# Kernel tuning notes

Measured on AMD Instinct MI355X. Metric: run time of the kernel, lower is better.

The kernel has to match this reference:

```python
import jax, jax.numpy as jnp
import numpy as np
import math

B, S, H, NH, NB = 2, 512, 128, 4, 2
D = H // NH
V_ITEMS, NCAT, NMETA, BAG, TSPAN = 50000, 1000, 16, 5, 256
EPS_EMB, EPS = 1e-5, 1e-8
NEG = -(2.0 ** 32) + 1.0


def _ln(x, g, b, eps):
    m = x.mean(-1, keepdims=True)
    v = ((x - m) ** 2).mean(-1, keepdims=True)
    return (x - m) / jnp.sqrt(v + eps) * g + b


def setup_inputs() -> dict:
    key = jax.random.key(0)
    ks = jax.random.split(key, 24)
    sc = 0.02
    inp = {}
    inp['input_ids'] = jax.random.randint(ks[0], (B, S), 0, V_ITEMS + 1)
    inp['metadata_seq'] = jax.random.normal(ks[1], (B, S, NMETA), jnp.float32)
    inp['category_seq'] = jax.random.randint(ks[2], (B, S, BAG), 0, NCAT + 1)
    inp['time_matrix'] = jax.random.randint(ks[3], (B, S, S), 0, TSPAN + 1)
    item = jax.random.normal(ks[4], (V_ITEMS + 1, H), jnp.float32) * sc
    inp['item_emb_w'] = item.at[0].set(0.0)  # padding_idx=0 cleared
    cat = jax.random.normal(ks[5], (NCAT + 1, H // 2), jnp.float32) * sc
    inp['cat_emb_w'] = cat.at[0].set(0.0)
    inp['num_W'] = jax.random.normal(ks[6], (H // 2, NMETA), jnp.float32) * sc
    inp['num_b'] = jnp.zeros((H // 2,), jnp.float32)
    inp['fusion_W'] = jax.random.normal(ks[7], (H, 2 * H), jnp.float32) * sc
    inp['fusion_b'] = jnp.zeros((H,), jnp.float32)
    inp['emb_ln_g'] = jnp.ones((H,), jnp.float32)
    inp['emb_ln_b'] = jnp.zeros((H,), jnp.float32)
    inp['pos_K_w'] = jax.random.normal(ks[8], (S, H), jnp.float32) * sc
    inp['pos_V_w'] = jax.random.normal(ks[9], (S, H), jnp.float32) * sc
    inp['time_K_w'] = jax.random.normal(ks[10], (TSPAN + 1, H), jnp.float32) * sc
    inp['time_V_w'] = jax.random.normal(ks[11], (TSPAN + 1, H), jnp.float32) * sc
    inp['attn_ln_g'] = jnp.ones((NB, H), jnp.float32)
    inp['attn_ln_b'] = jnp.zeros((NB, H), jnp.float32)
    inp['Q_W'] = jax.random.normal(ks[12], (NB, H, H), jnp.float32) * sc
    inp['Q_b'] = jnp.zeros((NB, H), jnp.float32)
    inp['K_W'] = jax.random.normal(ks[13], (NB, H, H), jnp.float32) * sc
    inp['K_b'] = jnp.zeros((NB, H), jnp.float32)
    inp['V_W'] = jax.random.normal(ks[14], (NB, H, H), jnp.float32) * sc
    inp['V_b'] = jnp.zeros((NB, H), jnp.float32)
    inp['fwd_ln_g'] = jnp.ones((NB, H), jnp.float32)
    inp['fwd_ln_b'] = jnp.zeros((NB, H), jnp.float32)
    inp['w1_W'] = jax.random.normal(ks[15], (NB, H, H), jnp.float32) * sc
    inp['w1_b'] = jnp.zeros((NB, H), jnp.float32)
    inp['w2_W'] = jax.random.normal(ks[16], (NB, H, H), jnp.float32) * sc
    inp['w2_b'] = jnp.zeros((NB, H), jnp.float32)
    inp['last_ln_g'] = jnp.ones((H,), jnp.float32)
    inp['last_ln_b'] = jnp.zeros((H,), jnp.float32)
    return inp


def reference(input_ids, metadata_seq, category_seq, time_matrix, item_emb_w,
              cat_emb_w, num_W, num_b, fusion_W, fusion_b, emb_ln_g, emb_ln_b,
              pos_K_w, pos_V_w, time_K_w, time_V_w, attn_ln_g, attn_ln_b,
              Q_W, Q_b, K_W, K_b, V_W, V_b, fwd_ln_g, fwd_ln_b,
              w1_W, w1_b, w2_W, w2_b, last_ln_g, last_ln_b):
    # ---- seq2vec ----
    item_v = item_emb_w[input_ids] * math.sqrt(H)            # [B,S,H]
    bag_mask = (category_seq != 0)                           # EmbeddingBag mean, padding_idx=0
    cat_e = cat_emb_w[category_seq] * bag_mask[..., None]    # [B,S,BAG,H/2]
    cat_v = cat_e.sum(-2) / jnp.maximum(bag_mask.sum(-1, keepdims=True), 1)
    num_v = metadata_seq @ num_W.T + num_b                   # [B,S,H/2]
    comb = jnp.concatenate([item_v, num_v, cat_v], axis=-1)  # [B,S,2H]
    vecs = _ln(comb @ fusion_W.T + fusion_b, emb_ln_g, emb_ln_b, EPS_EMB)

    # ---- vec2feats ----
    posK = pos_K_w.reshape(S, NH, D)
    posV = pos_V_w.reshape(S, NH, D)
    tK = time_K_w[time_matrix].reshape(B, S, S, NH, D)       # [B,S,S,h,d]
    tV = time_V_w[time_matrix].reshape(B, S, S, NH, D)
    timeline = (input_ids == 0)                              # [B,S]
    keep = (~timeline)[..., None].astype(vecs.dtype)
    vecs = vecs * keep
    causal = ~jnp.tril(jnp.ones((S, S), bool))               # mask where j > i
    inv_sqrt_d = 1.0 / math.sqrt(D)

    for i in range(NB):
        Qn = _ln(vecs, attn_ln_g[i], attn_ln_b[i], EPS)
        Q = (Qn @ Q_W[i].T + Q_b[i]).reshape(B, S, NH, D)
        K = (vecs @ K_W[i].T + K_b[i]).reshape(B, S, NH, D)
        V = (vecs @ V_W[i].T + V_b[i]).reshape(B, S, NH, D)
        aw = jnp.einsum('bihd,bjhd->bhij', Q, K)
        aw = aw + jnp.einsum('bihd,jhd->bhij', Q, posK)
        aw = aw + jnp.einsum('bijhd,bihd->bhij', tK, Q)
        aw = aw * inv_sqrt_d
        aw = jnp.where(timeline[:, None, :, None], NEG, aw)  # masks query rows (as in torch)
        aw = jnp.where(causal[None, None], NEG, aw)
        aw = jax.nn.softmax(aw, axis=-1)
        out = jnp.einsum('bhij,bjhd->bihd', aw, V)
        out = out + jnp.einsum('bhij,jhd->bihd', aw, posV)
        out = out + jnp.einsum('bhij,bijhd->bihd', aw, tV)
        out = out.reshape(B, S, H)
        vecs = Qn + out
        vecs = _ln(vecs, fwd_ln_g[i], fwd_ln_b[i], EPS)
        h1 = jax.nn.gelu(vecs @ w1_W[i].T + w1_b[i], approximate=False)
        vecs = vecs + (h1 @ w2_W[i].T + w2_b[i])
        vecs = vecs * keep

    return _ln(vecs, last_ln_g, last_ln_b, EPS)
```

## Files before the change

### kernel.cpp

```cpp
#include <hip/hip_runtime.h>
#include <math.h>

#define Bn 2
#define Sn 512
#define Hn 128
#define NHn 4
#define Dn 32
#define BAGn 5
#define NMETAn 16
#define ROWS 1024
#define NBn 2
#define Tt 257

#define NEGF (-4294967295.0f)
#define INV_SQRT_D 0.17677669529663687f
#define SQRT_H 11.313708498984761f
#define EPS_EMB 1e-5f
#define EPSF 1e-8f

#define OFF_QN    0
#define OFF_Q     131072
#define OFF_K     262144
#define OFF_V     393216
#define OFF_O     524288

static __device__ __forceinline__ float red64(float v) {
#pragma unroll
    for (int m = 1; m < 64; m <<= 1) v += __shfl_xor(v, m, 64);
    return v;
}
static __device__ __forceinline__ float red64max(float v) {
#pragma unroll
    for (int m = 1; m < 64; m <<= 1) v = fmaxf(v, __shfl_xor(v, m, 64));
    return v;
}
static __device__ __forceinline__ float dot4(float4 a, float4 b) {
    return a.x * b.x + a.y * b.y + a.z * b.z + a.w * b.w;
}
static __device__ __forceinline__ float red4(float v) {
    v += __shfl_xor(v, 1, 64);
    v += __shfl_xor(v, 2, 64);
    return v;
}

__global__ __launch_bounds__(256) void embed_qkv_kernel(
    const int* __restrict__ ids, const float* __restrict__ meta,
    const int* __restrict__ cats,
    const float* __restrict__ item_w, const float* __restrict__ cat_w,
    const float* __restrict__ numW, const float* __restrict__ numb,
    const float* __restrict__ fusW, const float* __restrict__ fusb,
    const float* __restrict__ elng, const float* __restrict__ elnb,
    const float* __restrict__ alng, const float* __restrict__ alnb,
    const float* __restrict__ QW, const float* __restrict__ Qb,
    const float* __restrict__ KW, const float* __restrict__ Kb,
    const float* __restrict__ VW, const float* __restrict__ Vb,
    const float* __restrict__ posK, const float* __restrict__ posV,
    const int* __restrict__ tmat, const float* __restrict__ tKw,
    const float* __restrict__ tVw,
    float* __restrict__ Qn, float* __restrict__ Q,
    float* __restrict__ K, float* __restrict__ V)
{
    int r0 = blockIdx.x * 2, t = threadIdx.x;
    __shared__ __align__(16) float combs[512];
    __shared__ __align__(16) float xs[256];
    __shared__ __align__(16) float qs[256];
    __shared__ float wsum[8];
    __shared__ int idl[2];

    int pfi = 0; float pff = 0.f;
    {
        const int* tm = tmat + blockIdx.x * 1024;
#pragma unroll
        for (int j = 0; j < 4; ++j) pfi += tm[t + j * 256];
        if (t < 64) {
            int off = blockIdx.x * 64 + t;
            pff = tKw[off] + tVw[off];
        } else if (blockIdx.x == 0 && t < 192) {
            pff = tKw[32704 + t] + tVw[32704 + t];
        }
    }

    if (t < 2) idl[t] = ids[r0 + t];
    __syncthreads();
    { int r = t >> 7, c = t & 127; combs[r * 256 + c] = item_w[idl[r] * Hn + c] * SQRT_H; }
    if (t < 128) {
        int r = t >> 6, c = t & 63;
        const float4* m4 = (const float4*)(meta + (r0 + r) * NMETAn);
        const float4* w4 = (const float4*)(numW + c * NMETAn);
        float acc = numb[c];
#pragma unroll
        for (int j = 0; j < 4; ++j) acc += dot4(m4[j], w4[j]);
        combs[r * 256 + 128 + c] = acc;
    } else {
        int u = t - 128, r = u >> 6, c = u & 63;
        float ca = 0.f; int cnt = 0;
#pragma unroll
        for (int k2 = 0; k2 < BAGn; ++k2) {
            int cc2 = cats[(r0 + r) * BAGn + k2];
            if (cc2 != 0) { ca += cat_w[cc2 * 64 + c]; cnt++; }
        }
        combs[r * 256 + 192 + c] = ca / (float)(cnt > 0 ? cnt : 1);
    }
    asm volatile("" :: "v"(pfi), "v"(pff));
    __syncthreads();

    int q = t & 3, g = t >> 2;
#pragma unroll
    for (int p = 0; p < 2; ++p) {
        int h = p * 64 + g;
        const float4* w4 = (const float4*)(fusW + h * 256) + q;
        const float4* c0 = (const float4*)(combs) + q;
        const float4* c1 = (const float4*)(combs + 256) + q;
        float a0 = 0.f, a1 = 0.f;
#pragma unroll
        for (int j = 0; j < 16; ++j) {
            float4 w = w4[j * 4];
            a0 += dot4(c0[j * 4], w);
            a1 += dot4(c1[j * 4], w);
        }
        a0 = red4(a0); a1 = red4(a1);
        if (q == 0)      xs[h]       = a0 + fusb[h];
        else if (q == 1) xs[128 + h] = a1 + fusb[h];
    }
    __syncthreads();

    int w_ = t >> 6, row = w_ >> 1, l = t & 63, ch = ((w_ & 1) << 6) + l;
    float x = xs[row * 128 + ch];
    float s1 = red64(x);
    if (l == 0) wsum[w_] = s1;
    __syncthreads();
    float mean = (wsum[row * 2] + wsum[row * 2 + 1]) * (1.f / 128.f);
    float dlt = x - mean;
    float s2 = red64(dlt * dlt);
    if (l == 0) wsum[4 + w_] = s2;
    __syncthreads();
    float rstd = rsqrtf((wsum[4 + row * 2] + wsum[4 + row * 2 + 1]) * (1.f / 128.f) + EPS_EMB);
    float xv = dlt * rstd * elng[ch] + elnb[ch];
    xv = (idl[row] == 0) ? 0.f : xv;
    __syncthreads();
    xs[row * 128 + ch] = xv;
    __syncthreads();
    s1 = red64(xv);
    if (l == 0) wsum[w_] = s1;
    __syncthreads();
    mean = (wsum[row * 2] + wsum[row * 2 + 1]) * (1.f / 128.f);
    dlt = xv - mean;
    s2 = red64(dlt * dlt);
    if (l == 0) wsum[4 + w_] = s2;
    __syncthreads();
    rstd = rsqrtf((wsum[4 + row * 2] + wsum[4 + row * 2 + 1]) * (1.f / 128.f) + EPSF);
    float qn = dlt * rstd * alng[ch] + alnb[ch];
    qs[row * 128 + ch] = qn;
    Qn[(r0 + row) * 128 + ch] = qn;
    __syncthreads();

#pragma unroll
    for (int p = 0; p < 2; ++p) {
        int h = p * 64 + g;
        const float4* qw = (const float4*)(QW + h * 128) + q;
        const float4* kw = (const float4*)(KW + h * 128) + q;
        const float4* vw = (const float4*)(VW + h * 128) + q;
        const float4* s0p = (const float4*)(qs) + q;
        const float4* s1p = (const float4*)(qs + 128) + q;
        const float4* x0p = (const float4*)(xs) + q;
        const float4* x1p = (const float4*)(xs + 128) + q;
        float aq0 = 0, aq1 = 0, ak0 = 0, ak1 = 0, av0 = 0, av1 = 0;
#pragma unroll
        for (int j = 0; j < 8; ++j) {
            float4 wq = qw[j * 4], wk = kw[j * 4], wv = vw[j * 4];
            float4 u0 = s0p[j * 4], u1 = s1p[j * 4];
            float4 y0 = x0p[j * 4], y1 = x1p[j * 4];
            aq0 += dot4(u0, wq); aq1 += dot4(u1, wq);
            ak0 += dot4(y0, wk); ak1 += dot4(y1, wk);
            av0 += dot4(y0, wv); av1 += dot4(y1, wv);
        }
        aq0 = red4(aq0); aq1 = red4(aq1);
        ak0 = red4(ak0); ak1 = red4(ak1);
        av0 = red4(av0); av1 = red4(av1);
        if (q == 0) {
            int si = r0 & (Sn - 1);
            Q[r0 * Hn + h] = aq0 + Qb[h];
            K[r0 * Hn + h] = ak0 + Kb[h] + posK[si * Hn + h];
            V[r0 * Hn + h] = av0 + Vb[h] + posV[si * Hn + h];
        } else if (q == 1) {
            int si = (r0 + 1) & (Sn - 1);
            Q[(r0 + 1) * Hn + h] = aq1 + Qb[h];
            K[(r0 + 1) * Hn + h] = ak1 + Kb[h] + posK[si * Hn + h];
            V[(r0 + 1) * Hn + h] = av1 + Vb[h] + posV[si * Hn + h];
        }
    }
}

static __device__ __forceinline__ void attn_phase(
    int b, int h, int i0, int t,
    const int* __restrict__ ids, const int* __restrict__ tmat,
    const float* __restrict__ Q, const float* __restrict__ K,
    const float* __restrict__ V,
    const float* __restrict__ tKw, const float* __restrict__ tVw,
    float* __restrict__ O,
    float* Kt, float* Vt, float* Stile, int* trowT,
    float* QTl, float* ql, int* tlf)
{
    if (t < 4) tlf[t] = (ids[b * Sn + i0 + t] == 0) ? 1 : 0;
    if (t < 128) {
        int q_ = t >> 5, d = t & 31;
        ql[q_ * 36 + d] = Q[(b * Sn + i0 + q_) * Hn + h * 32 + d];
    }
    __syncthreads();

    {
        int qq = t & 3, gg = t >> 2;
#pragma unroll
        for (int c = 0; c < 4; ++c) {
            int tt = c * 64 + gg;
            const float4* tk4 = (const float4*)(tKw + tt * Hn + h * 32);
            float4 wA = tk4[qq];
            float4 wB = tk4[qq + 4];
            int dA = qq * 4, dB = 16 + qq * 4;
            float a0 = ql[dA]*wA.x + ql[dA+1]*wA.y + ql[dA+2]*wA.z + ql[dA+3]*wA.w
                     + ql[dB]*wB.x + ql[dB+1]*wB.y + ql[dB+2]*wB.z + ql[dB+3]*wB.w;
            float a1 = ql[36+dA]*wA.x + ql[37+dA]*wA.y + ql[38+dA]*wA.z + ql[39+dA]*wA.w
                     + ql[36+dB]*wB.x + ql[37+dB]*wB.y + ql[38+dB]*wB.z + ql[39+dB]*wB.w;
            float a2 = ql[72+dA]*wA.x + ql[73+dA]*wA.y + ql[74+dA]*wA.z + ql[75+dA]*wA.w
                     + ql[72+dB]*wB.x + ql[73+dB]*wB.y + ql[74+dB]*wB.z + ql[75+dB]*wB.w;
            float a3 = ql[108+dA]*wA.x + ql[109+dA]*wA.y + ql[110+dA]*wA.z + ql[111+dA]*wA.w
                     + ql[108+dB]*wB.x + ql[109+dB]*wB.y + ql[110+dB]*wB.z + ql[111+dB]*wB.w;
            a0 = red4(a0); a1 = red4(a1); a2 = red4(a2); a3 = red4(a3);
            if (qq == 0)      QTl[tt] = a0;
            else if (qq == 1) QTl[260 + tt] = a1;
            else if (qq == 2) QTl[520 + tt] = a2;
            else              QTl[780 + tt] = a3;
        }
        if (t < 4) {
            const float4* tk4 = (const float4*)(tKw + 256 * Hn + h * 32);
            float4 wA = tk4[t];
            float4 wB = tk4[t + 4];
            int dA = t * 4, dB = 16 + t * 4;
            float a0 = ql[dA]*wA.x + ql[dA+1]*wA.y + ql[dA+2]*wA.z + ql[dA+3]*wA.w
                     + ql[dB]*wB.x + ql[dB+1]*wB.y + ql[dB+2]*wB.z + ql[dB+3]*wB.w;
            float a1 = ql[36+dA]*wA.x + ql[37+dA]*wA.y + ql[38+dA]*wA.z + ql[39+dA]*wA.w
                     + ql[36+dB]*wB.x + ql[37+dB]*wB.y + ql[38+dB]*wB.z + ql[39+dB]*wB.w;
            float a2 = ql[72+dA]*wA.x + ql[73+dA]*wA.y + ql[74+dA]*wA.z + ql[75+dA]*wA.w
                     + ql[72+dB]*wB.x + ql[73+dB]*wB.y + ql[74+dB]*wB.z + ql[75+dB]*wB.w;
            float a3 = ql[108+dA]*wA.x + ql[109+dA]*wA.y + ql[110+dA]*wA.z + ql[111+dA]*wA.w
                     + ql[108+dB]*wB.x + ql[109+dB]*wB.y + ql[110+dB]*wB.z + ql[111+dB]*wB.w;
            a0 = red4(a0); a1 = red4(a1); a2 = red4(a2); a3 = red4(a3);
            if (t == 0)      QTl[256] = a0;
            else if (t == 1) QTl[516] = a1;
            else if (t == 2) QTl[776] = a2;
            else             QTl[1036] = a3;
        }
    }

    int tl_any = tlf[0] | tlf[1] | tlf[2] | tlf[3];
    int ntiles = tl_any ? 8 : ((i0 + 3) >> 6) + 1;

    int iq = t >> 6, jj = t & 63;
    int i_g = i0 + iq;
    int my_tl = tlf[iq];
    const int* trow = tmat + (b * Sn + i_g) * Sn;

    float4 qv[8];
    {
        const float4* qp = (const float4*)(ql + iq * 36);
#pragma unroll
        for (int d = 0; d < 8; ++d) qv[d] = qp[d];
    }

    int jq = jj >> 5, d = jj & 31;
    float m = -INFINITY, lsum = 0.f, acc = 0.f;

    for (int jt = 0; jt < ntiles; ++jt) {
        int j0 = jt * 64;
        __syncthreads();
        for (int f = t; f < 64 * 8; f += 256) {
            int jl = f >> 3, dv = f & 7;
            float4 w4 = *(const float4*)(K + (b * Sn + j0 + jl) * Hn + h * 32 + dv * 4);
            *(float4*)(Kt + jl * 36 + dv * 4) = w4;
            float4 v4 = *(const float4*)(V + (b * Sn + j0 + jl) * Hn + h * 32 + dv * 4);
            *(float4*)(Vt + jl * 36 + dv * 4) = v4;
        }
        __syncthreads();

        int active = my_tl || (j0 <= i_g);
        if (active) {
            int j = j0 + jj;
            float sv = NEGF;
            int tv = trow[j];
            if (!my_tl && j <= i_g) {
                const float4* kr = (const float4*)(Kt + jj * 36);
                float a = 0.f;
#pragma unroll
                for (int dd = 0; dd < 8; ++dd)
                    a += dot4(qv[dd], kr[dd]);
                sv = (a + QTl[iq * 260 + tv]) * INV_SQRT_D;
            }
            float mt = red64max(sv);
            float mnew = fmaxf(m, mt);
            float alpha = expf(m - mnew);
            float p = expf(sv - mnew);
            lsum = lsum * alpha + red64(p);
            m = mnew;
            acc *= alpha;
            Stile[iq * 64 + jj] = p;
            trowT[iq * 64 + jj] = tv;
            int base = jq * 32;
#pragma unroll 8
            for (int jl = base; jl < base + 32; ++jl) {
                float pp = Stile[iq * 64 + jl];
                int tv2 = trowT[iq * 64 + jl];
                acc += pp * (Vt[jl * 36 + d] + tVw[tv2 * Hn + h * 32 + d]);
            }
        }
    }

    float a2 = acc + __shfl_xor(acc, 32, 64);
    if (jj < 32)
        O[(b * Sn + i_g) * Hn + h * 32 + d] = a2 / lsum;
}

__global__ __launch_bounds__(256) void attn_kernel(
    const int* ids, const int* tmat,
    const float* Q, const float* K, const float* V,
    const float* tKw, const float* tVw, float* O)
{
    __shared__ __align__(16) float Kt[64 * 36];
    __shared__ __align__(16) float Vt[64 * 36];
    __shared__ float Stile[4 * 64];
    __shared__ int   trowT[4 * 64];
    __shared__ float QTl[4 * 260];
    __shared__ __align__(16) float ql[4 * 36];
    __shared__ int tlf[4];
    int blk = blockIdx.x, t = threadIdx.x;
    int bh = blk & 7;
    int s  = blk >> 3;
    int g = s >> 5, r = s & 31;
    int mm;
    if      (g == 0) mm = r;
    else if (g == 1) mm = 127 - r;
    else if (g == 2) mm = 32 + r;
    else             mm = 95 - r;
    int b = bh >> 2, h = bh & 3;
    attn_phase(b, h, mm * 4, t, ids, tmat, Q, K, V, tKw, tVw, O,
               Kt, Vt, Stile, trowT, QTl, ql, tlf);
}

__global__ __launch_bounds__(256) void ffn_qkv_kernel(
    const int* __restrict__ ids, float* __restrict__ Qn,
    const float* __restrict__ O,
    const float* __restrict__ flng, const float* __restrict__ flnb,
    const float* __restrict__ w1W, const float* __restrict__ w1b,
    const float* __restrict__ w2W, const float* __restrict__ w2b,
    const float* __restrict__ alng, const float* __restrict__ alnb,
    const float* __restrict__ QW, const float* __restrict__ Qb,
    const float* __restrict__ KW, const float* __restrict__ Kb,
    const float* __restrict__ VW, const float* __restrict__ Vb,
    const float* __restrict__ posK, const float* __restrict__ posV,
    float* __restrict__ Q, float* __restrict__ K, float* __restrict__ V,
    const float* __restrict__ llng, const float* __restrict__ llnb,
    float* __restrict__ out, int nb, int last)
{
    int r0 = blockIdx.x * 2, t = threadIdx.x;
    __shared__ __align__(16) float ys[256];
    __shared__ __align__(16) float h1s[256];
    __shared__ float wsum[8];
    int id0 = ids[r0], id1 = ids[r0 + 1];

    ys[t] = Qn[r0 * 128 + t] + O[r0 * 128 + t];
    __syncthreads();
    int w_ = t >> 6, row = w_ >> 1, l = t & 63, ch = ((w_ & 1) << 6) + l;
    float x = ys[row * 128 + ch];
    float s1 = red64(x);
    if (l == 0) wsum[w_] = s1;
    __syncthreads();
    float mean = (wsum[row * 2] + wsum[row * 2 + 1]) * (1.f / 128.f);
    float dlt = x - mean;
    float s2 = red64(dlt * dlt);
    if (l == 0) wsum[4 + w_] = s2;
    __syncthreads();
    float rstd = rsqrtf((wsum[4 + row * 2] + wsum[4 + row * 2 + 1]) * (1.f / 128.f) + EPSF);
    float yv = dlt * rstd * flng[nb * 128 + ch] + flnb[nb * 128 + ch];
    __syncthreads();
    ys[row * 128 + ch] = yv;
    __syncthreads();

    int q = t & 3, g = t >> 2;
#pragma unroll
    for (int p = 0; p < 2; ++p) {
        int h = p * 64 + g;
        const float4* w4 = (const float4*)(w1W + nb * 16384 + h * 128) + q;
        const float4* y0 = (const float4*)(ys) + q;
        const float4* y1 = (const float4*)(ys + 128) + q;
        float a0 = 0.f, a1 = 0.f;
#pragma unroll
        for (int j = 0; j < 8; ++j) {
            float4 w = w4[j * 4];
            a0 += dot4(y0[j * 4], w);
            a1 += dot4(y1[j * 4], w);
        }
        a0 = red4(a0); a1 = red4(a1);
        if (q == 0) {
            float v0 = a0 + w1b[nb * 128 + h];
            h1s[h] = 0.5f * v0 * (1.f + erff(v0 * 0.70710678118654752f));
        } else if (q == 1) {
            float v1 = a1 + w1b[nb * 128 + h];
            h1s[128 + h] = 0.5f * v1 * (1.f + erff(v1 * 0.70710678118654752f));
        }
    }
    __syncthreads();

    float z00, z01, z10, z11;
    {
        float zz[2][2];
#pragma unroll
        for (int p = 0; p < 2; ++p) {
            int h = p * 64 + g;
            const float4* w4 = (const float4*)(w2W + nb * 16384 + h * 128) + q;
            const float4* y0 = (const float4*)(h1s) + q;
            const float4* y1 = (const float4*)(h1s + 128) + q;
            float a0 = 0.f, a1 = 0.f;
#pragma unroll
            for (int j = 0; j < 8; ++j) {
                float4 w = w4[j * 4];
                a0 += dot4(y0[j * 4], w);
                a1 += dot4(y1[j * 4], w);
            }
            a0 = red4(a0); a1 = red4(a1);
            float b_ = w2b[nb * 128 + h];
            zz[p][0] = (id0 == 0) ? 0.f : (a0 + b_ + ys[h]);
            zz[p][1] = (id1 == 0) ? 0.f : (a1 + b_ + ys[128 + h]);
        }
        z00 = zz[0][0]; z10 = zz[1][0]; z01 = zz[0][1]; z11 = zz[1][1];
    }
    __syncthreads();
    if (q == 0)      { h1s[g] = z00;        h1s[64 + g] = z10; }
    else if (q == 1) { h1s[128 + g] = z01;  h1s[192 + g] = z11; }
    __syncthreads();

    if (last) {
        x = h1s[row * 128 + ch];
        s1 = red64(x);
        if (l == 0) wsum[w_] = s1;
        __syncthreads();
        mean = (wsum[row * 2] + wsum[row * 2 + 1]) * (1.f / 128.f);
        dlt = x - mean;
        s2 = red64(dlt * dlt);
        if (l == 0) wsum[4 + w_] = s2;
        __syncthreads();
        rstd = rsqrtf((wsum[4 + row * 2] + wsum[4 + row * 2 + 1]) * (1.f / 128.f) + EPSF);
        out[(r0 + row) * 128 + ch] = dlt * rstd * llng[ch] + llnb[ch];
        return;
    }

    int nq = nb + 1;
    x = h1s[row * 128 + ch];
    s1 = red64(x);
    if (l == 0) wsum[w_] = s1;
    __syncthreads();
    mean = (wsum[row * 2] + wsum[row * 2 + 1]) * (1.f / 128.f);
    dlt = x - mean;
    s2 = red64(dlt * dlt);
    if (l == 0) wsum[4 + w_] = s2;
    __syncthreads();
    rstd = rsqrtf((wsum[4 + row * 2] + wsum[4 + row * 2 + 1]) * (1.f / 128.f) + EPSF);
    float qn = dlt * rstd * alng[nq * 128 + ch] + alnb[nq * 128 + ch];
    __syncthreads();
    ys[row * 128 + ch] = qn;
    Qn[(r0 + row) * 128 + ch] = qn;
    __syncthreads();

#pragma unroll
    for (int p = 0; p < 2; ++p) {
        int h = p * 64 + g;
        const float4* qw = (const float4*)(QW + nq * 16384 + h * 128) + q;
        const float4* kw = (const float4*)(KW + nq * 16384 + h * 128) + q;
        const float4* vw = (const float4*)(VW + nq * 16384 + h * 128) + q;
        const float4* s0p = (const float4*)(ys) + q;
        const float4* s1p = (const float4*)(ys + 128) + q;
        const float4* x0p = (const float4*)(h1s) + q;
        const float4* x1p = (const float4*)(h1s + 128) + q;
        float aq0 = 0, aq1 = 0, ak0 = 0, ak1 = 0, av0 = 0, av1 = 0;
#pragma unroll
        for (int j = 0; j < 8; ++j) {
            float4 wq = qw[j * 4], wk = kw[j * 4], wv = vw[j * 4];
            float4 u0 = s0p[j * 4], u1 = s1p[j * 4];
            float4 y0 = x0p[j * 4], y1 = x1p[j * 4];
            aq0 += dot4(u0, wq); aq1 += dot4(u1, wq);
            ak0 += dot4(y0, wk); ak1 += dot4(y1, wk);
            av0 += dot4(y0, wv); av1 += dot4(y1, wv);
        }
        aq0 = red4(aq0); aq1 = red4(aq1);
        ak0 = red4(ak0); ak1 = red4(ak1);
        av0 = red4(av0); av1 = red4(av1);
        if (q == 0) {
            int si = r0 & (Sn - 1);
            Q[r0 * Hn + h] = aq0 + Qb[nq * 128 + h];
            K[r0 * Hn + h] = ak0 + Kb[nq * 128 + h] + posK[si * Hn + h];
            V[r0 * Hn + h] = av0 + Vb[nq * 128 + h] + posV[si * Hn + h];
        } else if (q == 1) {
            int si = (r0 + 1) & (Sn - 1);
            Q[(r0 + 1) * Hn + h] = aq1 + Qb[nq * 128 + h];
            K[(r0 + 1) * Hn + h] = ak1 + Kb[nq * 128 + h] + posK[si * Hn + h];
            V[(r0 + 1) * Hn + h] = av1 + Vb[nq * 128 + h] + posV[si * Hn + h];
        }
    }
}

extern "C" void kernel_launch(void* const* d_in, const int* in_sizes, int n_in,
                              void* d_out, int out_size, void* d_ws, size_t ws_size,
                              hipStream_t stream) {
    const int*   ids   = (const int*)  d_in[0];
    const float* meta  = (const float*)d_in[1];
    const int*   cats  = (const int*)  d_in[2];
    const int*   tmat  = (const int*)  d_in[3];
    const float* itemw = (const float*)d_in[4];
    const float* catw  = (const float*)d_in[5];
    const float* numW  = (const float*)d_in[6];
    const float* numb  = (const float*)d_in[7];
    const float* fusW  = (const float*)d_in[8];
    const float* fusb  = (const float*)d_in[9];
    const float* elng  = (const float*)d_in[10];
    const float* elnb  = (const float*)d_in[11];
    const float* posK  = (const float*)d_in[12];
    const float* posV  = (const float*)d_in[13];
    const float* tKw   = (const float*)d_in[14];
    const float* tVw   = (const float*)d_in[15];
    const float* alng  = (const float*)d_in[16];
    const float* alnb  = (const float*)d_in[17];
    const float* QW    = (const float*)d_in[18];
    const float* Qb    = (const float*)d_in[19];
    const float* KW    = (const float*)d_in[20];
    const float* Kb    = (const float*)d_in[21];
    const float* VW    = (const float*)d_in[22];
    const float* Vb    = (const float*)d_in[23];
    const float* flng  = (const float*)d_in[24];
    const float* flnb  = (const float*)d_in[25];
    const float* w1W   = (const float*)d_in[26];
    const float* w1b   = (const float*)d_in[27];
    const float* w2W   = (const float*)d_in[28];
    const float* w2b   = (const float*)d_in[29];
    const float* llng  = (const float*)d_in[30];
    const float* llnb  = (const float*)d_in[31];
    (void)in_sizes; (void)n_in; (void)out_size; (void)ws_size;

    float* ws = (float*)d_ws;
    float* Qnp = ws + OFF_QN;
    float* Qp  = ws + OFF_Q;
    float* Kp  = ws + OFF_K;
    float* Vp  = ws + OFF_V;
    float* Op  = ws + OFF_O;
    float* outp = (float*)d_out;

    embed_qkv_kernel<<<ROWS / 2, 256, 0, stream>>>(
        ids, meta, cats, itemw, catw, numW, numb, fusW, fusb, elng, elnb,
        alng, alnb, QW, Qb, KW, Kb, VW, Vb, posK, posV, tmat, tKw, tVw,
        Qnp, Qp, Kp, Vp);
    for (int nb = 0; nb < NBn; ++nb) {
        attn_kernel<<<1024, 256, 0, stream>>>(ids, tmat, Qp, Kp, Vp, tKw, tVw, Op);
        ffn_qkv_kernel<<<ROWS / 2, 256, 0, stream>>>(
            ids, Qnp, Op, flng, flnb, w1W, w1b, w2W, w2b,
            alng, alnb, QW, Qb, KW, Kb, VW, Vb, posK, posV,
            Qp, Kp, Vp, llng, llnb, outp, nb, (nb == NBn - 1) ? 1 : 0);
    }
}
```

Baseline: 220.4 us.

## Use single-pass LayerNorm statistics and register-prefetch next K/V tile

LayerNorm passes now compute sum and sum of squares in one reduction round, using var = E[x^2]-mean^2. This removes several __syncthreads barriers and shared-memory round trips per block in the embedding and FFN kernels. The attention loop also prefetches the next K/V tile into registers while the current tile is consumed, hiding global load latency. The tradeoffs are reduced numerical robustness of the one-pass variance, which matters with EPS 1e-8, and higher register pressure.

```diff
diff --git a/kernel.cpp b/kernel.cpp
--- a/kernel.cpp
+++ b/kernel.cpp
@@ -64,7 +64,7 @@
     __shared__ __align__(16) float combs[512];
     __shared__ __align__(16) float xs[256];
     __shared__ __align__(16) float qs[256];
-    __shared__ float wsum[8];
+    __shared__ float wsum[16];
     __shared__ int idl[2];
 
     int pfi = 0; float pff = 0.f;
@@ -124,34 +124,28 @@
     }
     __syncthreads();
 
-    int w_ = t >> 6, row = w_ >> 1, l = t & 63, ch = ((w_ & 1) << 6) + l;
-    float x = xs[row * 128 + ch];
+    int row = t >> 7, ch = t & 127, w_ = t >> 6, l = t & 63;
+    float x = xs[t];
     float s1 = red64(x);
-    if (l == 0) wsum[w_] = s1;
+    float s2 = red64(x * x);
+    if (l == 0) { wsum[w_] = s1; wsum[4 + w_] = s2; }
     __syncthreads();
     float mean = (wsum[row * 2] + wsum[row * 2 + 1]) * (1.f / 128.f);
-    float dlt = x - mean;
-    float s2 = red64(dlt * dlt);
-    if (l == 0) wsum[4 + w_] = s2;
-    __syncthreads();
-    float rstd = rsqrtf((wsum[4 + row * 2] + wsum[4 + row * 2 + 1]) * (1.f / 128.f) + EPS_EMB);
-    float xv = dlt * rstd * elng[ch] + elnb[ch];
+    float ex2  = (wsum[4 + row * 2] + wsum[4 + row * 2 + 1]) * (1.f / 128.f);
+    float rstd = rsqrtf(ex2 - mean * mean + EPS_EMB);
+    float xv = (x - mean) * rstd * elng[ch] + elnb[ch];
     xv = (idl[row] == 0) ? 0.f : xv;
-    __syncthreads();
-    xs[row * 128 + ch] = xv;
-    __syncthreads();
+    xs[t] = xv;
     s1 = red64(xv);
-    if (l == 0) wsum[w_] = s1;
-    __syncthreads();
-    mean = (wsum[row * 2] + wsum[row * 2 + 1]) * (1.f / 128.f);
-    dlt = xv - mean;
-    s2 = red64(dlt * dlt);
-    if (l == 0) wsum[4 + w_] = s2;
-    __syncthreads();
-    rstd = rsqrtf((wsum[4 + row * 2] + wsum[4 + row * 2 + 1]) * (1.f / 128.f) + EPSF);
-    float qn = dlt * rstd * alng[ch] + alnb[ch];
-    qs[row * 128 + ch] = qn;
-    Qn[(r0 + row) * 128 + ch] = qn;
+    s2 = red64(xv * xv);
+    if (l == 0) { wsum[8 + w_] = s1; wsum[12 + w_] = s2; }
+    __syncthreads();
+    mean = (wsum[8 + row * 2] + wsum[8 + row * 2 + 1]) * (1.f / 128.f);
+    ex2  = (wsum[12 + row * 2] + wsum[12 + row * 2 + 1]) * (1.f / 128.f);
+    rstd = rsqrtf(ex2 - mean * mean + EPSF);
+    float qn = (xv - mean) * rstd * alng[ch] + alnb[ch];
+    qs[t] = qn;
+    Qn[r0 * 128 + t] = qn;
     __syncthreads();
 
 #pragma unroll
@@ -201,6 +195,15 @@
     float* Kt, float* Vt, float* Stile, int* trowT,
     float* QTl, float* ql, int* tlf)
 {
+    float4 kr[2], vr[2];
+#pragma unroll
+    for (int u = 0; u < 2; ++u) {
+        int f = t + u * 256;
+        int jl = f >> 3, dv = f & 7;
+        kr[u] = *(const float4*)(K + (size_t)(b * Sn + jl) * Hn + h * 32 + dv * 4);
+        vr[u] = *(const float4*)(V + (size_t)(b * Sn + jl) * Hn + h * 32 + dv * 4);
+    }
+
     if (t < 4) tlf[t] = (ids[b * Sn + i0 + t] == 0) ? 1 : 0;
     if (t < 128) {
         int q_ = t >> 5, d = t & 31;
@@ -273,14 +276,24 @@
     for (int jt = 0; jt < ntiles; ++jt) {
         int j0 = jt * 64;
         __syncthreads();
-        for (int f = t; f < 64 * 8; f += 256) {
+#pragma unroll
+        for (int u = 0; u < 2; ++u) {
+            int f = t + u * 256;
             int jl = f >> 3, dv = f & 7;
-            float4 w4 = *(const float4*)(K + (b * Sn + j0 + jl) * Hn + h * 32 + dv * 4);
-            *(float4*)(Kt + jl * 36 + dv * 4) = w4;
-            float4 v4 = *(const float4*)(V + (b * Sn + j0 + jl) * Hn + h * 32 + dv * 4);
-            *(float4*)(Vt + jl * 36 + dv * 4) = v4;
+            *(float4*)(Kt + jl * 36 + dv * 4) = kr[u];
+            *(float4*)(Vt + jl * 36 + dv * 4) = vr[u];
         }
         __syncthreads();
+        if (jt + 1 < ntiles) {
+            int j0n = (jt + 1) * 64;
+#pragma unroll
+            for (int u = 0; u < 2; ++u) {
+                int f = t + u * 256;
+                int jl = f >> 3, dv = f & 7;
+                kr[u] = *(const float4*)(K + (size_t)(b * Sn + j0n + jl) * Hn + h * 32 + dv * 4);
+                vr[u] = *(const float4*)(V + (size_t)(b * Sn + j0n + jl) * Hn + h * 32 + dv * 4);
+            }
+        }
 
         int active = my_tl || (j0 <= i_g);
         if (active) {
@@ -288,11 +301,11 @@
             float sv = NEGF;
             int tv = trow[j];
             if (!my_tl && j <= i_g) {
-                const float4* kr = (const float4*)(Kt + jj * 36);
+                const float4* kr4 = (const float4*)(Kt + jj * 36);
                 float a = 0.f;
 #pragma unroll
                 for (int dd = 0; dd < 8; ++dd)
-                    a += dot4(qv[dd], kr[dd]);
+                    a += dot4(qv[dd], kr4[dd]);
                 sv = (a + QTl[iq * 260 + tv]) * INV_SQRT_D;
             }
             float mt = red64max(sv);
@@ -363,25 +376,20 @@
     int r0 = blockIdx.x * 2, t = threadIdx.x;
     __shared__ __align__(16) float ys[256];
     __shared__ __align__(16) float h1s[256];
-    __shared__ float wsum[8];
+    __shared__ float wsum[16];
     int id0 = ids[r0], id1 = ids[r0 + 1];
 
-    ys[t] = Qn[r0 * 128 + t] + O[r0 * 128 + t];
-    __syncthreads();
-    int w_ = t >> 6, row = w_ >> 1, l = t & 63, ch = ((w_ & 1) << 6) + l;
-    float x = ys[row * 128 + ch];
+    int row = t >> 7, ch = t & 127, w_ = t >> 6, l = t & 63;
+    float x = Qn[r0 * 128 + t] + O[r0 * 128 + t];
     float s1 = red64(x);
-    if (l == 0) wsum[w_] = s1;
+    float s2 = red64(x * x);
+    if (l == 0) { wsum[w_] = s1; wsum[4 + w_] = s2; }
     __syncthreads();
     float mean = (wsum[row * 2] + wsum[row * 2 + 1]) * (1.f / 128.f);
-    float dlt = x - mean;
-    float s2 = red64(dlt * dlt);
-    if (l == 0) wsum[4 + w_] = s2;
-    __syncthreads();
-    float rstd = rsqrtf((wsum[4 + row * 2] + wsum[4 + row * 2 + 1]) * (1.f / 128.f) + EPSF);
-    float yv = dlt * rstd * flng[nb * 128 + ch] + flnb[nb * 128 + ch];
-    __syncthreads();
-    ys[row * 128 + ch] = yv;
+    float ex2  = (wsum[4 + row * 2] + wsum[4 + row * 2 + 1]) * (1.f / 128.f);
+    float rstd = rsqrtf(ex2 - mean * mean + EPSF);
+    float yv = (x - mean) * rstd * flng[nb * 128 + ch] + flnb[nb * 128 + ch];
+    ys[t] = yv;
     __syncthreads();
 
     int q = t & 3, g = t >> 2;
@@ -437,36 +445,24 @@
     else if (q == 1) { h1s[128 + g] = z01;  h1s[192 + g] = z11; }
     __syncthreads();
 
+    float zz2 = h1s[t];
+    s1 = red64(zz2);
+    s2 = red64(zz2 * zz2);
+    if (l == 0) { wsum[8 + w_] = s1; wsum[12 + w_] = s2; }
+    __syncthreads();
+    mean = (wsum[8 + row * 2] + wsum[8 + row * 2 + 1]) * (1.f / 128.f);
+    ex2  = (wsum[12 + row * 2] + wsum[12 + row * 2 + 1]) * (1.f / 128.f);
+    rstd = rsqrtf(ex2 - mean * mean + EPSF);
+
     if (last) {
-        x = h1s[row * 128 + ch];
-        s1 = red64(x);
-        if (l == 0) wsum[w_] = s1;
-        __syncthreads();
-        mean = (wsum[row * 2] + wsum[row * 2 + 1]) * (1.f / 128.f);
-        dlt = x - mean;
-        s2 = red64(dlt * dlt);
-        if (l == 0) wsum[4 + w_] = s2;
-        __syncthreads();
-        rstd = rsqrtf((wsum[4 + row * 2] + wsum[4 + row * 2 + 1]) * (1.f / 128.f) + EPSF);
-        out[(r0 + row) * 128 + ch] = dlt * rstd * llng[ch] + llnb[ch];
+        out[r0 * 128 + t] = (zz2 - mean) * rstd * llng[ch] + llnb[ch];
         return;
     }
 
     int nq = nb + 1;
-    x = h1s[row * 128 + ch];
-    s1 = red64(x);
-    if (l == 0) wsum[w_] = s1;
-    __syncthreads();
-    mean = (wsum[row * 2] + wsum[row * 2 + 1]) * (1.f / 128.f);
-    dlt = x - mean;
-    s2 = red64(dlt * dlt);
-    if (l == 0) wsum[4 + w_] = s2;
-    __syncthreads();
-    rstd = rsqrtf((wsum[4 + row * 2] + wsum[4 + row * 2 + 1]) * (1.f / 128.f) + EPSF);
-    float qn = dlt * rstd * alng[nq * 128 + ch] + alnb[nq * 128 + ch];
-    __syncthreads();
-    ys[row * 128 + ch] = qn;
-    Qn[(r0 + row) * 128 + ch] = qn;
+    float qn = (zz2 - mean) * rstd * alng[nq * 128 + ch] + alnb[nq * 128 + ch];
+    ys[t] = qn;
+    Qn[r0 * 128 + t] = qn;
     __syncthreads();
 
 #pragma unroll
```

New measurement: 252.6 us. +14.6%, slower.

## Process eight query rows per attention block, two per wavefront

Applied to the files above, without the earlier changes.

The attention kernel now handles 8 query rows per block instead of 4, with each wavefront processing two rows that share the same K/V tile staged in shared memory. The grid halves to 512 blocks, so K/V tiles are loaded from global memory half as often, and the per-query time-key projection setup covers more rows per block. The load-balancing order of row groups is simplified to a two-way mirror pairing, and a launch-bounds occupancy hint is added. In exchange, each wave does twice the serial work, there are fewer blocks to spread across CUs, and causal-tile imbalance within a block may grow.

```diff
diff --git a/kernel.cpp b/kernel.cpp
--- a/kernel.cpp
+++ b/kernel.cpp
@@ -191,135 +191,7 @@
     }
 }
 
-static __device__ __forceinline__ void attn_phase(
-    int b, int h, int i0, int t,
-    const int* __restrict__ ids, const int* __restrict__ tmat,
-    const float* __restrict__ Q, const float* __restrict__ K,
-    const float* __restrict__ V,
-    const float* __restrict__ tKw, const float* __restrict__ tVw,
-    float* __restrict__ O,
-    float* Kt, float* Vt, float* Stile, int* trowT,
-    float* QTl, float* ql, int* tlf)
-{
-    if (t < 4) tlf[t] = (ids[b * Sn + i0 + t] == 0) ? 1 : 0;
-    if (t < 128) {
-        int q_ = t >> 5, d = t & 31;
-        ql[q_ * 36 + d] = Q[(b * Sn + i0 + q_) * Hn + h * 32 + d];
-    }
-    __syncthreads();
-
-    {
-        int qq = t & 3, gg = t >> 2;
-#pragma unroll
-        for (int c = 0; c < 4; ++c) {
-            int tt = c * 64 + gg;
-            const float4* tk4 = (const float4*)(tKw + tt * Hn + h * 32);
-            float4 wA = tk4[qq];
-            float4 wB = tk4[qq + 4];
-            int dA = qq * 4, dB = 16 + qq * 4;
-            float a0 = ql[dA]*wA.x + ql[dA+1]*wA.y + ql[dA+2]*wA.z + ql[dA+3]*wA.w
-                     + ql[dB]*wB.x + ql[dB+1]*wB.y + ql[dB+2]*wB.z + ql[dB+3]*wB.w;
-            float a1 = ql[36+dA]*wA.x + ql[37+dA]*wA.y + ql[38+dA]*wA.z + ql[39+dA]*wA.w
-                     + ql[36+dB]*wB.x + ql[37+dB]*wB.y + ql[38+dB]*wB.z + ql[39+dB]*wB.w;
-            float a2 = ql[72+dA]*wA.x + ql[73+dA]*wA.y + ql[74+dA]*wA.z + ql[75+dA]*wA.w
-                     + ql[72+dB]*wB.x + ql[73+dB]*wB.y + ql[74+dB]*wB.z + ql[75+dB]*wB.w;
-            float a3 = ql[108+dA]*wA.x + ql[109+dA]*wA.y + ql[110+dA]*wA.z + ql[111+dA]*wA.w
-                     + ql[108+dB]*wB.x + ql[109+dB]*wB.y + ql[110+dB]*wB.z + ql[111+dB]*wB.w;
-            a0 = red4(a0); a1 = red4(a1); a2 = red4(a2); a3 = red4(a3);
-            if (qq == 0)      QTl[tt] = a0;
-            else if (qq == 1) QTl[260 + tt] = a1;
-            else if (qq == 2) QTl[520 + tt] = a2;
-            else              QTl[780 + tt] = a3;
-        }
-        if (t < 4) {
-            const float4* tk4 = (const float4*)(tKw + 256 * Hn + h * 32);
-            float4 wA = tk4[t];
-            float4 wB = tk4[t + 4];
-            int dA = t * 4, dB = 16 + t * 4;
-            float a0 = ql[dA]*wA.x + ql[dA+1]*wA.y + ql[dA+2]*wA.z + ql[dA+3]*wA.w
-                     + ql[dB]*wB.x + ql[dB+1]*wB.y + ql[dB+2]*wB.z + ql[dB+3]*wB.w;
-            float a1 = ql[36+dA]*wA.x + ql[37+dA]*wA.y + ql[38+dA]*wA.z + ql[39+dA]*wA.w
-                     + ql[36+dB]*wB.x + ql[37+dB]*wB.y + ql[38+dB]*wB.z + ql[39+dB]*wB.w;
-            float a2 = ql[72+dA]*wA.x + ql[73+dA]*wA.y + ql[74+dA]*wA.z + ql[75+dA]*wA.w
-                     + ql[72+dB]*wB.x + ql[73+dB]*wB.y + ql[74+dB]*wB.z + ql[75+dB]*wB.w;
-            float a3 = ql[108+dA]*wA.x + ql[109+dA]*wA.y + ql[110+dA]*wA.z + ql[111+dA]*wA.w
-                     + ql[108+dB]*wB.x + ql[109+dB]*wB.y + ql[110+dB]*wB.z + ql[111+dB]*wB.w;
-            a0 = red4(a0); a1 = red4(a1); a2 = red4(a2); a3 = red4(a3);
-            if (t == 0)      QTl[256] = a0;
-            else if (t == 1) QTl[516] = a1;
-            else if (t == 2) QTl[776] = a2;
-            else             QTl[1036] = a3;
-        }
-    }
-
-    int tl_any = tlf[0] | tlf[1] | tlf[2] | tlf[3];
-    int ntiles = tl_any ? 8 : ((i0 + 3) >> 6) + 1;
-
-    int iq = t >> 6, jj = t & 63;
-    int i_g = i0 + iq;
-    int my_tl = tlf[iq];
-    const int* trow = tmat + (b * Sn + i_g) * Sn;
-
-    float4 qv[8];
-    {
-        const float4* qp = (const float4*)(ql + iq * 36);
-#pragma unroll
-        for (int d = 0; d < 8; ++d) qv[d] = qp[d];
-    }
-
-    int jq = jj >> 5, d = jj & 31;
-    float m = -INFINITY, lsum = 0.f, acc = 0.f;
-
-    for (int jt = 0; jt < ntiles; ++jt) {
-        int j0 = jt * 64;
-        __syncthreads();
-        for (int f = t; f < 64 * 8; f += 256) {
-            int jl = f >> 3, dv = f & 7;
-            float4 w4 = *(const float4*)(K + (b * Sn + j0 + jl) * Hn + h * 32 + dv * 4);
-            *(float4*)(Kt + jl * 36 + dv * 4) = w4;
-            float4 v4 = *(const float4*)(V + (b * Sn + j0 + jl) * Hn + h * 32 + dv * 4);
-            *(float4*)(Vt + jl * 36 + dv * 4) = v4;
-        }
-        __syncthreads();
-
-        int active = my_tl || (j0 <= i_g);
-        if (active) {
-            int j = j0 + jj;
-            float sv = NEGF;
-            int tv = trow[j];
-            if (!my_tl && j <= i_g) {
-                const float4* kr = (const float4*)(Kt + jj * 36);
-                float a = 0.f;
-#pragma unroll
-                for (int dd = 0; dd < 8; ++dd)
-                    a += dot4(qv[dd], kr[dd]);
-                sv = (a + QTl[iq * 260 + tv]) * INV_SQRT_D;
-            }
-            float mt = red64max(sv);
-            float mnew = fmaxf(m, mt);
-            float alpha = expf(m - mnew);
-            float p = expf(sv - mnew);
-            lsum = lsum * alpha + red64(p);
-            m = mnew;
-            acc *= alpha;
-            Stile[iq * 64 + jj] = p;
-            trowT[iq * 64 + jj] = tv;
-            int base = jq * 32;
-#pragma unroll 8
-            for (int jl = base; jl < base + 32; ++jl) {
-                float pp = Stile[iq * 64 + jl];
-                int tv2 = trowT[iq * 64 + jl];
-                acc += pp * (Vt[jl * 36 + d] + tVw[tv2 * Hn + h * 32 + d]);
-            }
-        }
-    }
-
-    float a2 = acc + __shfl_xor(acc, 32, 64);
-    if (jj < 32)
-        O[(b * Sn + i_g) * Hn + h * 32 + d] = a2 / lsum;
-}
-
-__global__ __launch_bounds__(256) void attn_kernel(
+__global__ __launch_bounds__(256, 2) void attn_kernel(
     const int* ids, const int* tmat,
     const float* Q, const float* K, const float* V,
     const float* tKw, const float* tVw, float* O)
@@ -328,21 +200,144 @@
     __shared__ __align__(16) float Vt[64 * 36];
     __shared__ float Stile[4 * 64];
     __shared__ int   trowT[4 * 64];
-    __shared__ float QTl[4 * 260];
-    __shared__ __align__(16) float ql[4 * 36];
-    __shared__ int tlf[4];
+    __shared__ float QTl[8 * 260];
+    __shared__ __align__(16) float ql[8 * 36];
+    __shared__ int tlf[8];
+
     int blk = blockIdx.x, t = threadIdx.x;
     int bh = blk & 7;
     int s  = blk >> 3;
-    int g = s >> 5, r = s & 31;
-    int mm;
-    if      (g == 0) mm = r;
-    else if (g == 1) mm = 127 - r;
-    else if (g == 2) mm = 32 + r;
-    else             mm = 95 - r;
+    int g  = (s < 32) ? s : 95 - s;
     int b = bh >> 2, h = bh & 3;
-    attn_phase(b, h, mm * 4, t, ids, tmat, Q, K, V, tKw, tVw, O,
-               Kt, Vt, Stile, trowT, QTl, ql, tlf);
+    int i0 = g * 8;
+
+    if (t < 8) tlf[t] = (ids[b * Sn + i0 + t] == 0) ? 1 : 0;
+    { int q_ = t >> 5, d = t & 31;
+      ql[q_ * 36 + d] = Q[(b * Sn + i0 + q_) * Hn + h * 32 + d]; }
+    __syncthreads();
+
+    {
+        int qq = t & 3, gg = t >> 2;
+#pragma unroll
+        for (int c = 0; c < 5; ++c) {
+            int tt = c * 64 + gg;
+            if (tt < Tt) {
+                const float4* tk4 = (const float4*)(tKw + tt * Hn + h * 32);
+                float4 wA = tk4[qq];
+                float4 wB = tk4[qq + 4];
+                int dA = qq * 4, dB = 16 + qq * 4;
+#pragma unroll
+                for (int qi = 0; qi < 8; ++qi) {
+                    const float* r_ = ql + qi * 36;
+                    float a = r_[dA]*wA.x + r_[dA+1]*wA.y + r_[dA+2]*wA.z + r_[dA+3]*wA.w
+                            + r_[dB]*wB.x + r_[dB+1]*wB.y + r_[dB+2]*wB.z + r_[dB+3]*wB.w;
+                    a = red4(a);
+                    if (qq == (qi & 3)) QTl[qi * 260 + tt] = a;
+                }
+            }
+        }
+    }
+
+    int tl_any = 0;
+#pragma unroll
+    for (int i = 0; i < 8; ++i) tl_any |= tlf[i];
+    int ntiles = tl_any ? 8 : ((i0 + 7) >> 6) + 1;
+
+    int w = t >> 6, jj = t & 63;
+    int q0 = w * 2;
+    int i_g0 = i0 + q0, i_g1 = i0 + q0 + 1;
+    int tl0 = tlf[q0], tl1 = tlf[q0 + 1];
+    const int* trow0 = tmat + (size_t)(b * Sn + i_g0) * Sn;
+    const int* trow1 = tmat + (size_t)(b * Sn + i_g1) * Sn;
+
+    float4 qa[8], qb[8];
+    {
+        const float4* p0 = (const float4*)(ql + q0 * 36);
+        const float4* p1 = (const float4*)(ql + (q0 + 1) * 36);
+#pragma unroll
+        for (int d = 0; d < 8; ++d) { qa[d] = p0[d]; qb[d] = p1[d]; }
+    }
+
+    int jq = jj >> 5, d = jj & 31;
+    float m0 = -INFINITY, l0 = 0.f, a0 = 0.f;
+    float m1 = -INFINITY, l1 = 0.f, a1 = 0.f;
+
+    for (int jt = 0; jt < ntiles; ++jt) {
+        int j0 = jt * 64;
+        __syncthreads();
+        for (int f = t; f < 512; f += 256) {
+            int jl = f >> 3, dv = f & 7;
+            float4 w4 = *(const float4*)(K + (size_t)(b * Sn + j0 + jl) * Hn + h * 32 + dv * 4);
+            *(float4*)(Kt + jl * 36 + dv * 4) = w4;
+            float4 v4 = *(const float4*)(V + (size_t)(b * Sn + j0 + jl) * Hn + h * 32 + dv * 4);
+            *(float4*)(Vt + jl * 36 + dv * 4) = v4;
+        }
+        __syncthreads();
+
+        if (tl0 || j0 <= i_g0) {
+            int j = j0 + jj;
+            float sv = NEGF;
+            int tv = trow0[j];
+            if (!tl0 && j <= i_g0) {
+                const float4* kr = (const float4*)(Kt + jj * 36);
+                float a = 0.f;
+#pragma unroll
+                for (int dd = 0; dd < 8; ++dd) a += dot4(qa[dd], kr[dd]);
+                sv = (a + QTl[q0 * 260 + tv]) * INV_SQRT_D;
+            }
+            float mt = red64max(sv);
+            float mnew = fmaxf(m0, mt);
+            float alpha = expf(m0 - mnew);
+            float p = expf(sv - mnew);
+            l0 = l0 * alpha + red64(p);
+            m0 = mnew;
+            a0 *= alpha;
+            Stile[w * 64 + jj] = p;
+            trowT[w * 64 + jj] = tv;
+            int base = jq * 32;
+#pragma unroll 8
+            for (int jl = base; jl < base + 32; ++jl) {
+                float pp = Stile[w * 64 + jl];
+                int tv2 = trowT[w * 64 + jl];
+                a0 += pp * (Vt[jl * 36 + d] + tVw[tv2 * Hn + h * 32 + d]);
+            }
+        }
+        if (tl1 || j0 <= i_g1) {
+            int j = j0 + jj;
+            float sv = NEGF;
+            int tv = trow1[j];
+            if (!tl1 && j <= i_g1) {
+                const float4* kr = (const float4*)(Kt + jj * 36);
+                float a = 0.f;
+#pragma unroll
+                for (int dd = 0; dd < 8; ++dd) a += dot4(qb[dd], kr[dd]);
+                sv = (a + QTl[(q0 + 1) * 260 + tv]) * INV_SQRT_D;
+            }
+            float mt = red64max(sv);
+            float mnew = fmaxf(m1, mt);
+            float alpha = expf(m1 - mnew);
+            float p = expf(sv - mnew);
+            l1 = l1 * alpha + red64(p);
+            m1 = mnew;
+            a1 *= alpha;
+            Stile[w * 64 + jj] = p;
+            trowT[w * 64 + jj] = tv;
+            int base = jq * 32;
+#pragma unroll 8
+            for (int jl = base; jl < base + 32; ++jl) {
+                float pp = Stile[w * 64 + jl];
+                int tv2 = trowT[w * 64 + jl];
+                a1 += pp * (Vt[jl * 36 + d] + tVw[tv2 * Hn + h * 32 + d]);
+            }
+        }
+    }
+
+    float o0 = a0 + __shfl_xor(a0, 32, 64);
+    float o1 = a1 + __shfl_xor(a1, 32, 64);
+    if (jj < 32) {
+        O[(size_t)(b * Sn + i_g0) * Hn + h * 32 + d] = o0 / l0;
+        O[(size_t)(b * Sn + i_g1) * Hn + h * 32 + d] = o1 / l1;
+    }
 }
 
 __global__ __launch_bounds__(256) void ffn_qkv_kernel(
@@ -556,7 +551,7 @@
         alng, alnb, QW, Qb, KW, Kb, VW, Vb, posK, posV, tmat, tKw, tVw,
         Qnp, Qp, Kp, Vp);
     for (int nb = 0; nb < NBn; ++nb) {
-        attn_kernel<<<1024, 256, 0, stream>>>(ids, tmat, Qp, Kp, Vp, tKw, tVw, Op);
+        attn_kernel<<<512, 256, 0, stream>>>(ids, tmat, Qp, Kp, Vp, tKw, tVw, Op);
         ffn_qkv_kernel<<<ROWS / 2, 256, 0, stream>>>(
             ids, Qnp, Op, flng, flnb, w1W, w1b, w2W, w2b,
             alng, alnb, QW, Qb, KW, Kb, VW, Vb, posK, posV,
```

Result: slower. 249.7 us (+13.3%).
